# Optimization experiments

Hardware: AMD Instinct MI355X
Metric: run time of the kernel (lower is better)

Reference implementation:

```python
import jax, jax.numpy as jnp
import numpy as np
from jax import lax

BATCH = 2
COUNT = 5
OUT = 125


def _bins(n, out=OUT):
    # PyTorch adaptive_max_pool2d bin boundaries: start=floor(i*n/out), end=ceil((i+1)*n/out)
    i = np.arange(out)
    s = (i * n) // out
    e = -((-(i + 1) * n) // out)
    m = int((e - s).max())
    idx = s[:, None] + np.arange(m)[None, :]
    return np.minimum(idx, n - 1), idx < e[:, None]


def _apool(img):
    # adaptive max pool 2d of [H,W] -> [OUT,OUT]; H,W are concrete Python ints
    H, W = img.shape
    ri, rv = _bins(H)
    ci, cv = _bins(W)
    r = jnp.where(rv[:, :, None], img[ri], -jnp.inf).max(axis=1)       # [OUT, W]
    return jnp.where(cv[None], r[:, ci], -jnp.inf).max(axis=2)         # [OUT, OUT]


def _conv(x, w, b):
    y = lax.conv_general_dilated(x, w, (1, 1), 'VALID', dimension_numbers=('NCHW', 'OIHW', 'NCHW'))
    return y + b[None, :, None, None]


def _bn(x, g, be, m, v):
    inv = g * lax.rsqrt(v + 1e-5)
    return x * inv[None, :, None, None] + (be - m * inv)[None, :, None, None]


def _pool(x, k, s):
    return lax.reduce_window(x, -np.inf, lax.max, (1, 1, k, k), (1, 1, s, s), 'VALID')


def _forward(x, ROI, roi_layer, w1, b1, g1, be1, m1, v1, w2, b2, g2, be2, m2, v2,
             w3, b3, g3, be3, m3, v3, w4, b4, g4, be4, m4, v4, fw1, fb1, fw2, fb2, fw3, fb3):
    ROI = np.asarray(ROI)
    rl = int(roi_layer)
    roiX = jax.nn.relu(_bn(_conv(x, w1, b1), g1, be1, m1, v1))  # [2,3,252,252]
    crops = []
    for k in range(BATCH):
        xs = []
        for j in range(rl):
            for i in range(COUNT):
                y1, y2, x1, x2 = (int(v) for v in ROI[k, i, 0])
                y1 = int(y1 * 0.9); y2 = int(y2 * 0.9); x2 = int(x2 * 0.9); x1 = int(x1 * 0.9)
                xs.append(_apool(roiX[k, j, y1:y2, x1:x2]))
        crops.append(xs)
    # original code prepends each batch's crop list -> batch order reversed; .numpy() detaches grads
    xb = lax.stop_gradient(jnp.stack(crops[1] + crops[0]).reshape(BATCH, COUNT * rl, OUT, OUT))
    norX = _pool(jax.nn.relu(_bn(_conv(x, w2, b2), g2, be2, m2, v2)), 4, 2)  # [2,20,125,125]
    h = jnp.concatenate([norX, xb], axis=1)                                   # [2,35,125,125]
    h = _pool(jax.nn.relu(_bn(_conv(h, w3, b3), g3, be3, m3, v3)), 2, 2)      # [2,50,60,60]
    h = _pool(jax.nn.relu(_bn(_conv(h, w4, b4), g4, be4, m4, v4)), 2, 2)      # [2,25,28,28]
    h = h.reshape(BATCH, -1)                                                  # [2,19600]
    h = jax.nn.relu(h @ fw1 + fb1)
    h = jax.nn.relu(h @ fw2 + fb2)
    h = jax.nn.relu(h @ fw3 + fb3)
    return jax.nn.softmax(h, axis=1)


def setup_inputs() -> dict:
    key = jax.random.key(0)
    ks = jax.random.split(key, 8)
    rng = np.random.default_rng(0)
    y1 = rng.integers(0, 100, (BATCH, COUNT))
    y2 = np.minimum(y1 + rng.integers(60, 150, (BATCH, COUNT)), 251)
    x1 = rng.integers(0, 100, (BATCH, COUNT))
    x2 = np.minimum(x1 + rng.integers(60, 150, (BATCH, COUNT)), 251)
    ROI = jnp.asarray(np.stack([y1, y2, x1, x2], -1)[:, :, None, :].astype(np.int32))
    d = {'x': jax.random.normal(ks[0], (BATCH, 1, 256, 256), jnp.float32), 'ROI': ROI, 'roi_layer': 3}
    d.update(w1=jax.random.normal(ks[1], (3, 1, 5, 5)) * 0.05, b1=jnp.zeros(3), g1=jnp.ones(3), be1=jnp.zeros(3), m1=jnp.zeros(3), v1=jnp.ones(3))
    d.update(w2=jax.random.normal(ks[2], (20, 1, 5, 5)) * 0.05, b2=jnp.zeros(20), g2=jnp.ones(20), be2=jnp.zeros(20), m2=jnp.zeros(20), v2=jnp.ones(20))
    d.update(w3=jax.random.normal(ks[3], (50, 35, 5, 5)) * 0.05, b3=jnp.zeros(50), g3=jnp.ones(50), be3=jnp.zeros(50), m3=jnp.zeros(50), v3=jnp.ones(50))
    d.update(w4=jax.random.normal(ks[4], (25, 50, 5, 5)) * 0.05, b4=jnp.zeros(25), g4=jnp.ones(25), be4=jnp.zeros(25), m4=jnp.zeros(25), v4=jnp.ones(25))
    d.update(fw1=jax.random.normal(ks[5], (25 * 28 * 28, 1024)) * 0.01, fb1=jnp.zeros(1024),
             fw2=jax.random.normal(ks[6], (1024, 32)) * 0.05, fb2=jnp.zeros(32),
             fw3=jax.random.normal(ks[7], (32, 2)) * 0.05, fb3=jnp.zeros(2))
    return d


def reference(x, ROI, roi_layer, w1, b1, g1, be1, m1, v1, w2, b2, g2, be2, m2, v2,
              w3, b3, g3, be3, m3, v3, w4, b4, g4, be4, m4, v4, fw1, fb1, fw2, fb2, fw3, fb3):
    return _forward(x, ROI, roi_layer, w1, b1, g1, be1, m1, v1, w2, b2, g2, be2, m2, v2,
                    w3, b3, g3, be3, m3, v3, w4, b4, g4, be4, m4, v4, fw1, fb1, fw2, fb2, fw3, fb3)
```

## Files before the change

### kernel.cpp

```cpp
#include <hip/hip_runtime.h>
#include <math.h>


#define RL 3
#define NCH 35

__global__ __launch_bounds__(256) void conv2_roi(
    const float* __restrict__ x, const int* __restrict__ ROI,
    const float* __restrict__ w2, const float* __restrict__ b2, const float* __restrict__ g2,
    const float* __restrict__ be2, const float* __restrict__ m2, const float* __restrict__ v2,
    const float* __restrict__ w1, const float* __restrict__ b1, const float* __restrict__ g1,
    const float* __restrict__ be1, const float* __restrict__ m1, const float* __restrict__ v1,
    const float* __restrict__ w3, const float* __restrict__ w4,
    float* __restrict__ wp3, float* __restrict__ wp4,
    float* __restrict__ h1) {
    if (blockIdx.y >= 70) {
        const float* src = (blockIdx.y == 70) ? w3 : w4;
        float* dst = (blockIdx.y == 70) ? wp3 : wp4;
        int rows = (blockIdx.y == 70) ? 50 * 35 : 25 * 50;
        int total = rows * 28;
        for (int i = blockIdx.x * 256 + threadIdx.x; i < total; i += gridDim.x * 256) {
            int t = i % 28, r = i / 28;
            dst[i] = (t < 25) ? src[r * 25 + t] : 0.f;
        }
        return;
    }
    int i = blockIdx.x * 256 + threadIdx.x;
    if (i >= 125 * 125) return;
    int oy = i / 125, ox = i % 125;
    if (blockIdx.y < 40) {
        int c = blockIdx.y % 20;
        int bi = blockIdx.y / 20;
        const float* xp = x + bi * 256 * 256 + (2 * oy) * 256 + 2 * ox;
        float wl[25];
#pragma unroll
        for (int k = 0; k < 25; k++) wl[k] = w2[c * 25 + k];
        float in[8][8];
#pragma unroll
        for (int r = 0; r < 8; r++)
#pragma unroll
            for (int k = 0; k < 4; k++) {
                float2 v2v = *(const float2*)(xp + r * 256 + 2 * k);
                in[r][2 * k] = v2v.x;
                in[r][2 * k + 1] = v2v.y;
            }
        float inv = g2[c] * rsqrtf(v2[c] + 1e-5f);
        float sh = (b2[c] - m2[c]) * inv + be2[c];
        float mx = -INFINITY;
#pragma unroll
        for (int py = 0; py < 4; py++) {
#pragma unroll
            for (int px = 0; px < 4; px++) {
                float acc = 0.f;
#pragma unroll
                for (int ky = 0; ky < 5; ky++)
#pragma unroll
                    for (int kx = 0; kx < 5; kx++)
                        acc = fmaf(in[py + ky][px + kx], wl[ky * 5 + kx], acc);
                mx = fmaxf(mx, fmaxf(acc * inv + sh, 0.f));
            }
        }
        h1[((bi * NCH + c) * 125 + oy) * 125 + ox] = mx;
    } else {
        int yz = blockIdx.y - 40;
        int bi = yz / 15;
        int cc = yz % 15;
        int sb = 1 - bi;
        int j = cc / 5;
        int ri = cc % 5;
        const int* rp = ROI + (sb * 5 + ri) * 4;
        int y1 = (9 * rp[0]) / 10;
        int y2 = (9 * rp[1]) / 10;
        int x1 = (9 * rp[2]) / 10;
        int x2 = (9 * rp[3]) / 10;
        int H = y2 - y1;
        int W = x2 - x1;
        int sy = (oy * H) / 125, ey = ((oy + 1) * H + 124) / 125;
        int sx = (ox * W) / 125, ex = ((ox + 1) * W + 124) / 125;
        float wl[25];
#pragma unroll
        for (int k = 0; k < 25; k++) wl[k] = w1[j * 25 + k];
        float inv = g1[j] * rsqrtf(v1[j] + 1e-5f);
        float sh = (b1[j] - m1[j]) * inv + be1[j];
        const float* xp = x + sb * 256 * 256;
        float mx = -INFINITY;
        for (int r = sy; r < ey; r++) {
            for (int c2 = sx; c2 < ex; c2++) {
                int Y = y1 + r, X = x1 + c2;
                float acc = 0.f;
#pragma unroll
                for (int ky = 0; ky < 5; ky++)
#pragma unroll
                    for (int kx = 0; kx < 5; kx++)
                        acc = fmaf(xp[(Y + ky) * 256 + X + kx], wl[ky * 5 + kx], acc);
                mx = fmaxf(mx, fmaxf(acc * inv + sh, 0.f));
            }
        }
        h1[((bi * NCH + 20 + cc) * 125 + oy) * 125 + ox] = mx;
    }
}

template <int IW, int PO, int CI, int CO, int G, int NG, int NS>
__global__ __launch_bounds__(64, 4) void conv_partial(
    const float* __restrict__ in, const float* __restrict__ wp,
    float* __restrict__ pac) {
    __shared__ float tile[2][20][24];

    const int lane = threadIdx.x;
    const int sy = lane >> 3, sx = lane & 7;
    int z = blockIdx.z;
    const int ng = z % NG; z /= NG;
    const int s = z % NS;
    const int bi = z / NS;
    const int co0 = ng * G;
    constexpr int CPS = (CI + NS - 1) / NS;
    const int ci0 = s * CPS;
    const int ci1 = (ci0 + CPS < CI) ? ci0 + CPS : CI;
    const int px0 = (8 * (int)blockIdx.x < PO - 8) ? 8 * (int)blockIdx.x : PO - 8;
    const int py0 = (8 * (int)blockIdx.y < PO - 8) ? 8 * (int)blockIdx.y : PO - 8;
    const int px = px0 + sx, py = py0 + sy;
    const float* ip = in + (size_t)bi * CI * IW * IW + (size_t)(2 * py0) * IW + 2 * px0;

    int cw[G];
#pragma unroll
    for (int gg = 0; gg < G; gg++) cw[gg] = (co0 + gg < CO) ? co0 + gg : CO - 1;

    float2 sreg[4];
    auto loadstage = [&](int ci) {
        const float* src = ip + (size_t)ci * IW * IW;
#pragma unroll
        for (int k = 0; k < 4; k++) {
            int p = lane + k * 64;
            if (p < 200) {
                int r = p / 10, c2 = (p % 10) * 2;
                sreg[k] = *(const float2*)(src + r * IW + c2);
            }
        }
    };
    auto writestage = [&](int buf) {
#pragma unroll
        for (int k = 0; k < 4; k++) {
            int p = lane + k * 64;
            if (p < 200) {
                int r = p / 10, c2 = (p % 10) * 2;
                *(float2*)&tile[buf][r][c2] = sreg[k];
            }
        }
    };

    float4 wA[7], wB[7];
    auto wload = [&](float4(&wr)[7], int gg, int ci) {
        const float* src = wp + ((size_t)cw[gg] * CI + ci) * 28;
#pragma unroll
        for (int k = 0; k < 7; k++) wr[k] = *(const float4*)(src + 4 * k);
    };

    float acc[G][4];
#pragma unroll
    for (int gg = 0; gg < G; gg++)
#pragma unroll
        for (int q = 0; q < 4; q++) acc[gg][q] = 0.f;

#define WE(W, t) ((t) % 4 == 0 ? W[(t) / 4].x : (t) % 4 == 1 ? W[(t) / 4].y : (t) % 4 == 2 ? W[(t) / 4].z : W[(t) / 4].w)
#define FMAG(W, gg)                                                            \
    {                                                                          \
        _Pragma("unroll") for (int ky = 0; ky < 5; ky++) {                     \
            _Pragma("unroll") for (int kx = 0; kx < 5; kx++) {                 \
                float wv = WE(W, ky * 5 + kx);                                 \
                float e00 = ((kx)&1) ? p[ky][kx >> 1].y : p[ky][kx >> 1].x;    \
                float e01 = ((kx + 1) & 1) ? p[ky][(kx + 1) >> 1].y : p[ky][(kx + 1) >> 1].x; \
                float e10 = ((kx)&1) ? p[ky + 1][kx >> 1].y : p[ky + 1][kx >> 1].x; \
                float e11 = ((kx + 1) & 1) ? p[ky + 1][(kx + 1) >> 1].y : p[ky + 1][(kx + 1) >> 1].x; \
                acc[gg][0] = fmaf(e00, wv, acc[gg][0]);                        \
                acc[gg][1] = fmaf(e01, wv, acc[gg][1]);                        \
                acc[gg][2] = fmaf(e10, wv, acc[gg][2]);                        \
                acc[gg][3] = fmaf(e11, wv, acc[gg][3]);                        \
            }                                                                  \
        }                                                                      \
    }

    loadstage(ci0);
    writestage(0);

    for (int ci = ci0; ci < ci1; ci++) {
        const int cur = (ci - ci0) & 1;
        if (ci + 1 < ci1) loadstage(ci + 1);
        wload(wA, 0, ci);
        float2 p[6][3];
#pragma unroll
        for (int r = 0; r < 6; r++)
#pragma unroll
            for (int c = 0; c < 3; c++)
                p[r][c] = *(const float2*)&tile[cur][2 * sy + r][2 * sx + 2 * c];
        wload(wB, 1, ci);
        FMAG(wA, 0);
        wload(wA, 2, ci);
        FMAG(wB, 1);
        FMAG(wA, 2);
        if (ci + 1 < ci1) writestage(cur ^ 1);
    }
#undef FMAG
#undef WE

    constexpr int CW = 2 * PO;
#pragma unroll
    for (int gg = 0; gg < G; gg++) {
        int co = co0 + gg;
        if (co < CO) {
            size_t base = (((size_t)(s * 2 + bi) * CO + co) * CW + 2 * py) * CW + 2 * px;
            float2 r0 = {acc[gg][0], acc[gg][1]};
            float2 r1 = {acc[gg][2], acc[gg][3]};
            *(float2*)&pac[base] = r0;
            *(float2*)&pac[base + CW] = r1;
        }
    }
}

template <int PO, int CO, int INIT>
__global__ __launch_bounds__(256) void conv_finish(
    const float* __restrict__ pac,
    const float* __restrict__ b, const float* __restrict__ g,
    const float* __restrict__ be, const float* __restrict__ m,
    const float* __restrict__ v, float* __restrict__ out,
    const float* __restrict__ fb1, float* __restrict__ fc1o) {
    int idx = blockIdx.x * 256 + threadIdx.x;
    if (INIT && idx < 2048) fc1o[idx] = fb1[idx & 1023];
    int total = 2 * CO * PO * PO;
    if (idx >= total) return;
    int px = idx % PO;
    int t = idx / PO;
    int py = t % PO; t /= PO;
    int co = t % CO;
    int bi = t / CO;
    constexpr int CW = 2 * PO;
    constexpr size_t SS = (size_t)2 * CO * CW * CW;
    size_t base = (((size_t)bi * CO + co) * CW + 2 * py) * CW + 2 * px;
    float s00 = 0.f, s01 = 0.f, s10 = 0.f, s11 = 0.f;
#pragma unroll
    for (int s = 0; s < 4; s++) {
        float2 a0 = *(const float2*)&pac[base + s * SS];
        float2 a1 = *(const float2*)&pac[base + s * SS + CW];
        s00 += a0.x; s01 += a0.y; s10 += a1.x; s11 += a1.y;
    }
    float inv = g[co] * rsqrtf(v[co] + 1e-5f);
    float sh = (b[co] - m[co]) * inv + be[co];
    float q0 = fmaxf(s00 * inv + sh, 0.f);
    float q1 = fmaxf(s01 * inv + sh, 0.f);
    float q2 = fmaxf(s10 * inv + sh, 0.f);
    float q3 = fmaxf(s11 * inv + sh, 0.f);
    out[idx] = fmaxf(fmaxf(q0, q1), fmaxf(q2, q3));
}

#define CHUNK 50
__global__ void fc1_mm(const float* __restrict__ h, const float* __restrict__ w,
                       float* __restrict__ out) {
    __shared__ float sh[2][CHUNK];
    int o = blockIdx.x * 256 + threadIdx.x;
    int i0 = blockIdx.y * CHUNK;
    if (threadIdx.x < 2 * CHUNK) {
        int r = threadIdx.x / CHUNK, t = threadIdx.x % CHUNK;
        sh[r][t] = h[r * 19600 + i0 + t];
    }
    __syncthreads();
    float a0 = 0.f, a1 = 0.f;
    const float* wp = w + (size_t)i0 * 1024 + o;
#pragma unroll
    for (int i = 0; i < CHUNK; i++) {
        float wv = wp[(size_t)i * 1024];
        a0 = fmaf(sh[0][i], wv, a0);
        a1 = fmaf(sh[1][i], wv, a1);
    }
    atomicAdd(&out[o], a0);
    atomicAdd(&out[1024 + o], a1);
}

__global__ void head(const float* __restrict__ fc1o, const float* __restrict__ fw2,
                     const float* __restrict__ fb2, const float* __restrict__ fw3,
                     const float* __restrict__ fb3, float* __restrict__ out) {
    int bi = blockIdx.x;
    __shared__ float h[1024];
    __shared__ float red[256];
    __shared__ float s2[32];
    for (int i = threadIdx.x; i < 1024; i += 256) h[i] = fmaxf(fc1o[bi * 1024 + i], 0.f);
    __syncthreads();
    int o = threadIdx.x >> 3;
    int part = threadIdx.x & 7;
    float a = 0.f;
    for (int i = part * 128; i < part * 128 + 128; i++) a += h[i] * fw2[i * 32 + o];
    red[threadIdx.x] = a;
    __syncthreads();
    if (part == 0) {
        float s = 0.f;
        for (int p = 0; p < 8; p++) s += red[(o << 3) + p];
        s2[o] = fmaxf(s + fb2[o], 0.f);
    }
    __syncthreads();
    if (threadIdx.x == 0) {
        float z0 = fb3[0], z1 = fb3[1];
        for (int i = 0; i < 32; i++) {
            z0 += s2[i] * fw3[i * 2];
            z1 += s2[i] * fw3[i * 2 + 1];
        }
        z0 = fmaxf(z0, 0.f);
        z1 = fmaxf(z1, 0.f);
        float mx = fmaxf(z0, z1);
        float e0 = expf(z0 - mx), e1 = expf(z1 - mx);
        float s = e0 + e1;
        out[bi * 2 + 0] = e0 / s;
        out[bi * 2 + 1] = e1 / s;
    }
}

extern "C" void kernel_launch(void* const* d_in, const int* in_sizes, int n_in,
                              void* d_out, int out_size, void* d_ws, size_t ws_size,
                              hipStream_t stream) {
    const float* x   = (const float*)d_in[0];
    const int*   ROI = (const int*)d_in[1];
    const float* w1 = (const float*)d_in[3];
    const float* b1 = (const float*)d_in[4];
    const float* g1 = (const float*)d_in[5];
    const float* be1 = (const float*)d_in[6];
    const float* m1 = (const float*)d_in[7];
    const float* v1 = (const float*)d_in[8];
    const float* w2 = (const float*)d_in[9];
    const float* b2 = (const float*)d_in[10];
    const float* g2 = (const float*)d_in[11];
    const float* be2 = (const float*)d_in[12];
    const float* m2 = (const float*)d_in[13];
    const float* v2 = (const float*)d_in[14];
    const float* w3 = (const float*)d_in[15];
    const float* b3 = (const float*)d_in[16];
    const float* g3 = (const float*)d_in[17];
    const float* be3 = (const float*)d_in[18];
    const float* m3 = (const float*)d_in[19];
    const float* v3 = (const float*)d_in[20];
    const float* w4 = (const float*)d_in[21];
    const float* b4 = (const float*)d_in[22];
    const float* g4 = (const float*)d_in[23];
    const float* be4 = (const float*)d_in[24];
    const float* m4 = (const float*)d_in[25];
    const float* v4 = (const float*)d_in[26];
    const float* fw1 = (const float*)d_in[27];
    const float* fb1 = (const float*)d_in[28];
    const float* fw2 = (const float*)d_in[29];
    const float* fb2 = (const float*)d_in[30];
    const float* fw3 = (const float*)d_in[31];
    const float* fb3 = (const float*)d_in[32];
    float* out = (float*)d_out;

    float* ws = (float*)d_ws;
    float* h1   = ws;
    float* p3   = h1 + 1093750;
    float* p4   = p3 + 360000;
    float* fc1o = p4 + 39200;
    float* pac3 = fc1o + 2048;
    float* pac4 = pac3;
    float* wp3  = pac3 + 5760000;
    float* wp4  = wp3 + 49000;

    {
        dim3 grd((125 * 125 + 255) / 256, 72);
        conv2_roi<<<grd, 256, 0, stream>>>(x, ROI, w2, b2, g2, be2, m2, v2,
                                           w1, b1, g1, be1, m1, v1,
                                           w3, w4, wp3, wp4, h1);
    }
    {
        dim3 grd(8, 8, 2 * 4 * 17);
        conv_partial<125, 60, NCH, 50, 3, 17, 4><<<grd, 64, 0, stream>>>(h1, wp3, pac3);
    }
    {
        int total = 2 * 50 * 60 * 60;
        conv_finish<60, 50, 0><<<(total + 255) / 256, 256, 0, stream>>>(
            pac3, b3, g3, be3, m3, v3, p3, nullptr, nullptr);
    }
    {
        dim3 grd(4, 4, 2 * 4 * 9);
        conv_partial<60, 28, 50, 25, 3, 9, 4><<<grd, 64, 0, stream>>>(p3, wp4, pac4);
    }
    {
        int total = 2 * 25 * 28 * 28;
        conv_finish<28, 25, 1><<<(total + 255) / 256, 256, 0, stream>>>(
            pac4, b4, g4, be4, m4, v4, p4, fb1, fc1o);
    }
    {
        dim3 grd(4, 392);
        fc1_mm<<<grd, 256, 0, stream>>>(p4, fw1, fc1o);
    }
    head<<<2, 256, 0, stream>>>(fc1o, fw2, fb2, fw3, fb3, out);
}
```

Baseline: 125.3 us.

## Pad h1 channel stride and software-pipeline conv_partial weight loads across channels

```diff
diff --git a/kernel.cpp b/kernel.cpp
--- a/kernel.cpp
+++ b/kernel.cpp
@@ -4,6 +4,8 @@
 
 #define RL 3
 #define NCH 35
+#define H1C 15626
+#define H1B (35 * H1C)
 
 __global__ __launch_bounds__(256) void conv2_roi(
     const float* __restrict__ x, const int* __restrict__ ROI,
@@ -60,7 +62,7 @@
                 mx = fmaxf(mx, fmaxf(acc * inv + sh, 0.f));
             }
         }
-        h1[((bi * NCH + c) * 125 + oy) * 125 + ox] = mx;
+        h1[(size_t)bi * H1B + (size_t)c * H1C + oy * 125 + ox] = mx;
     } else {
         int yz = blockIdx.y - 40;
         int bi = yz / 15;
@@ -96,12 +98,12 @@
                 mx = fmaxf(mx, fmaxf(acc * inv + sh, 0.f));
             }
         }
-        h1[((bi * NCH + 20 + cc) * 125 + oy) * 125 + ox] = mx;
-    }
-}
-
-template <int IW, int PO, int CI, int CO, int G, int NG, int NS>
-__global__ __launch_bounds__(64, 4) void conv_partial(
+        h1[(size_t)bi * H1B + (size_t)(20 + cc) * H1C + oy * 125 + ox] = mx;
+    }
+}
+
+template <int IW, int PO, int CI, int CO, int G, int NG, int NS, int BST, int CST>
+__global__ __launch_bounds__(64) void conv_partial(
     const float* __restrict__ in, const float* __restrict__ wp,
     float* __restrict__ pac) {
     __shared__ float tile[2][20][24];
@@ -119,7 +121,7 @@
     const int px0 = (8 * (int)blockIdx.x < PO - 8) ? 8 * (int)blockIdx.x : PO - 8;
     const int py0 = (8 * (int)blockIdx.y < PO - 8) ? 8 * (int)blockIdx.y : PO - 8;
     const int px = px0 + sx, py = py0 + sy;
-    const float* ip = in + (size_t)bi * CI * IW * IW + (size_t)(2 * py0) * IW + 2 * px0;
+    const float* ip = in + (size_t)bi * BST + (size_t)(2 * py0) * IW + 2 * px0;
 
     int cw[G];
 #pragma unroll
@@ -127,7 +129,7 @@
 
     float2 sreg[4];
     auto loadstage = [&](int ci) {
-        const float* src = ip + (size_t)ci * IW * IW;
+        const float* src = ip + (size_t)ci * CST;
 #pragma unroll
         for (int k = 0; k < 4; k++) {
             int p = lane + k * 64;
@@ -150,7 +152,8 @@
 
     float4 wA[7], wB[7];
     auto wload = [&](float4(&wr)[7], int gg, int ci) {
-        const float* src = wp + ((size_t)cw[gg] * CI + ci) * 28;
+        int cc = (ci < ci1) ? ci : ci1 - 1;
+        const float* src = wp + ((size_t)cw[gg] * CI + cc) * 28;
 #pragma unroll
         for (int k = 0; k < 7; k++) wr[k] = *(const float4*)(src + 4 * k);
     };
@@ -178,27 +181,42 @@
             }                                                                  \
         }                                                                      \
     }
+#define PREAD(buf)                                                             \
+    float2 p[6][3];                                                            \
+    _Pragma("unroll") for (int r = 0; r < 6; r++)                              \
+        _Pragma("unroll") for (int c = 0; c < 3; c++)                          \
+            p[r][c] = *(const float2*)&tile[buf][2 * sy + r][2 * sx + 2 * c];
 
     loadstage(ci0);
     writestage(0);
-
-    for (int ci = ci0; ci < ci1; ci++) {
-        const int cur = (ci - ci0) & 1;
-        if (ci + 1 < ci1) loadstage(ci + 1);
-        wload(wA, 0, ci);
-        float2 p[6][3];
-#pragma unroll
-        for (int r = 0; r < 6; r++)
-#pragma unroll
-            for (int c = 0; c < 3; c++)
-                p[r][c] = *(const float2*)&tile[cur][2 * sy + r][2 * sx + 2 * c];
-        wload(wB, 1, ci);
-        FMAG(wA, 0);
-        wload(wA, 2, ci);
-        FMAG(wB, 1);
-        FMAG(wA, 2);
-        if (ci + 1 < ci1) writestage(cur ^ 1);
-    }
+    wload(wA, 0, ci0);
+
+#pragma unroll 1
+    for (int ci = ci0; ci < ci1; ci += 2) {
+        {
+            if (ci + 1 < ci1) loadstage(ci + 1);
+            PREAD(0)
+            wload(wB, 1, ci);
+            FMAG(wA, 0);
+            wload(wA, 2, ci);
+            FMAG(wB, 1);
+            wload(wB, 0, ci + 1);
+            FMAG(wA, 2);
+            if (ci + 1 < ci1) writestage(1);
+        }
+        if (ci + 1 < ci1) {
+            if (ci + 2 < ci1) loadstage(ci + 2);
+            PREAD(1)
+            wload(wA, 1, ci + 1);
+            FMAG(wB, 0);
+            wload(wB, 2, ci + 1);
+            FMAG(wA, 1);
+            wload(wA, 0, ci + 2);
+            FMAG(wB, 2);
+            if (ci + 2 < ci1) writestage(0);
+        }
+    }
+#undef PREAD
 #undef FMAG
 #undef WE
 
@@ -350,7 +368,7 @@
 
     float* ws = (float*)d_ws;
     float* h1   = ws;
-    float* p3   = h1 + 1093750;
+    float* p3   = h1 + 2 * H1B;
     float* p4   = p3 + 360000;
     float* fc1o = p4 + 39200;
     float* pac3 = fc1o + 2048;
@@ -366,7 +384,8 @@
     }
     {
         dim3 grd(8, 8, 2 * 4 * 17);
-        conv_partial<125, 60, NCH, 50, 3, 17, 4><<<grd, 64, 0, stream>>>(h1, wp3, pac3);
+        conv_partial<125, 60, NCH, 50, 3, 17, 4, H1B, H1C><<<grd, 64, 0, stream>>>(
+            h1, wp3, pac3);
     }
     {
         int total = 2 * 50 * 60 * 60;
@@ -375,7 +394,8 @@
     }
     {
         dim3 grd(4, 4, 2 * 4 * 9);
-        conv_partial<60, 28, 50, 25, 3, 9, 4><<<grd, 64, 0, stream>>>(p3, wp4, pac4);
+        conv_partial<60, 28, 50, 25, 3, 9, 4, 180000, 3600><<<grd, 64, 0, stream>>>(
+            p3, wp4, pac4);
     }
     {
         int total = 2 * 25 * 28 * 28;
```

After: 125.8 us. About the same (+0.4%).

## Prefetch next-channel weights across conv iterations and pad h1 channel stride

Applied to the files above, without the earlier changes.

```diff
diff --git a/kernel.cpp b/kernel.cpp
--- a/kernel.cpp
+++ b/kernel.cpp
@@ -4,6 +4,8 @@
 
 #define RL 3
 #define NCH 35
+#define H1C 15626
+#define H1B (35 * H1C)
 
 __global__ __launch_bounds__(256) void conv2_roi(
     const float* __restrict__ x, const int* __restrict__ ROI,
@@ -60,7 +62,7 @@
                 mx = fmaxf(mx, fmaxf(acc * inv + sh, 0.f));
             }
         }
-        h1[((bi * NCH + c) * 125 + oy) * 125 + ox] = mx;
+        h1[(size_t)bi * H1B + (size_t)c * H1C + oy * 125 + ox] = mx;
     } else {
         int yz = blockIdx.y - 40;
         int bi = yz / 15;
@@ -96,14 +98,15 @@
                 mx = fmaxf(mx, fmaxf(acc * inv + sh, 0.f));
             }
         }
-        h1[((bi * NCH + 20 + cc) * 125 + oy) * 125 + ox] = mx;
-    }
-}
-
-template <int IW, int PO, int CI, int CO, int G, int NG, int NS>
-__global__ __launch_bounds__(64, 4) void conv_partial(
+        h1[(size_t)bi * H1B + (size_t)(20 + cc) * H1C + oy * 125 + ox] = mx;
+    }
+}
+
+template <int IW, int PO, int CI, int CO, int G, int NG, int NS, int BST, int CST>
+__global__ __launch_bounds__(64) void conv_partial(
     const float* __restrict__ in, const float* __restrict__ wp,
     float* __restrict__ pac) {
+    static_assert(G == 3, "schedule hard-coded for G=3");
     __shared__ float tile[2][20][24];
 
     const int lane = threadIdx.x;
@@ -119,7 +122,7 @@
     const int px0 = (8 * (int)blockIdx.x < PO - 8) ? 8 * (int)blockIdx.x : PO - 8;
     const int py0 = (8 * (int)blockIdx.y < PO - 8) ? 8 * (int)blockIdx.y : PO - 8;
     const int px = px0 + sx, py = py0 + sy;
-    const float* ip = in + (size_t)bi * CI * IW * IW + (size_t)(2 * py0) * IW + 2 * px0;
+    const float* ip = in + (size_t)bi * BST + (size_t)(2 * py0) * IW + 2 * px0;
 
     int cw[G];
 #pragma unroll
@@ -127,7 +130,7 @@
 
     float2 sreg[4];
     auto loadstage = [&](int ci) {
-        const float* src = ip + (size_t)ci * IW * IW;
+        const float* src = ip + (size_t)ci * CST;
 #pragma unroll
         for (int k = 0; k < 4; k++) {
             int p = lane + k * 64;
@@ -148,9 +151,10 @@
         }
     };
 
-    float4 wA[7], wB[7];
+    float4 wA[7], wB[7], wC[7];
     auto wload = [&](float4(&wr)[7], int gg, int ci) {
-        const float* src = wp + ((size_t)cw[gg] * CI + ci) * 28;
+        int cc = (ci < ci1) ? ci : ci1 - 1;
+        const float* src = wp + ((size_t)cw[gg] * CI + cc) * 28;
 #pragma unroll
         for (int k = 0; k < 7; k++) wr[k] = *(const float4*)(src + 4 * k);
     };
@@ -181,23 +185,31 @@
 
     loadstage(ci0);
     writestage(0);
-
+    wload(wA, 0, ci0);
+    wload(wB, 1, ci0);
+    wload(wC, 2, ci0);
+
+#pragma unroll 1
     for (int ci = ci0; ci < ci1; ci++) {
         const int cur = (ci - ci0) & 1;
-        if (ci + 1 < ci1) loadstage(ci + 1);
-        wload(wA, 0, ci);
+        const bool more = (ci + 1 < ci1);
+        if (more) loadstage(ci + 1);
         float2 p[6][3];
 #pragma unroll
         for (int r = 0; r < 6; r++)
 #pragma unroll
             for (int c = 0; c < 3; c++)
                 p[r][c] = *(const float2*)&tile[cur][2 * sy + r][2 * sx + 2 * c];
-        wload(wB, 1, ci);
         FMAG(wA, 0);
-        wload(wA, 2, ci);
+        if (more) wload(wA, 0, ci + 1);
+        __builtin_amdgcn_sched_barrier(0);
         FMAG(wB, 1);
-        FMAG(wA, 2);
-        if (ci + 1 < ci1) writestage(cur ^ 1);
+        if (more) wload(wB, 1, ci + 1);
+        __builtin_amdgcn_sched_barrier(0);
+        FMAG(wC, 2);
+        if (more) wload(wC, 2, ci + 1);
+        __builtin_amdgcn_sched_barrier(0);
+        if (more) writestage(cur ^ 1);
     }
 #undef FMAG
 #undef WE
@@ -350,7 +362,7 @@
 
     float* ws = (float*)d_ws;
     float* h1   = ws;
-    float* p3   = h1 + 1093750;
+    float* p3   = h1 + 2 * H1B;
     float* p4   = p3 + 360000;
     float* fc1o = p4 + 39200;
     float* pac3 = fc1o + 2048;
@@ -366,7 +378,8 @@
     }
     {
         dim3 grd(8, 8, 2 * 4 * 17);
-        conv_partial<125, 60, NCH, 50, 3, 17, 4><<<grd, 64, 0, stream>>>(h1, wp3, pac3);
+        conv_partial<125, 60, NCH, 50, 3, 17, 4, H1B, H1C><<<grd, 64, 0, stream>>>(
+            h1, wp3, pac3);
     }
     {
         int total = 2 * 50 * 60 * 60;
@@ -375,7 +388,8 @@
     }
     {
         dim3 grd(4, 4, 2 * 4 * 9);
-        conv_partial<60, 28, 50, 25, 3, 9, 4><<<grd, 64, 0, stream>>>(p3, wp4, pac4);
+        conv_partial<60, 28, 50, 25, 3, 9, 4, 180000, 3600><<<grd, 64, 0, stream>>>(
+            p3, wp4, pac4);
     }
     {
         int total = 2 * 25 * 28 * 28;
```

Result: slower. 193.0 us (+54.1%).

## Fuse conv4 finish into fc1 and retune conv4 output-channel grouping

Applied to the files above, without the earlier changes.

```diff
diff --git a/kernel.cpp b/kernel.cpp
--- a/kernel.cpp
+++ b/kernel.cpp
@@ -100,10 +100,11 @@
     }
 }
 
-template <int IW, int PO, int CI, int CO, int G, int NG, int NS>
+template <int IW, int PO, int CI, int CO, int G, int NG, int NS, int BST, int CST>
 __global__ __launch_bounds__(64, 4) void conv_partial(
     const float* __restrict__ in, const float* __restrict__ wp,
     float* __restrict__ pac) {
+    static_assert(G == 2 || G == 3, "schedule supports G=2,3");
     __shared__ float tile[2][20][24];
 
     const int lane = threadIdx.x;
@@ -119,7 +120,7 @@
     const int px0 = (8 * (int)blockIdx.x < PO - 8) ? 8 * (int)blockIdx.x : PO - 8;
     const int py0 = (8 * (int)blockIdx.y < PO - 8) ? 8 * (int)blockIdx.y : PO - 8;
     const int px = px0 + sx, py = py0 + sy;
-    const float* ip = in + (size_t)bi * CI * IW * IW + (size_t)(2 * py0) * IW + 2 * px0;
+    const float* ip = in + (size_t)bi * BST + (size_t)(2 * py0) * IW + 2 * px0;
 
     int cw[G];
 #pragma unroll
@@ -127,7 +128,7 @@
 
     float2 sreg[4];
     auto loadstage = [&](int ci) {
-        const float* src = ip + (size_t)ci * IW * IW;
+        const float* src = ip + (size_t)ci * CST;
 #pragma unroll
         for (int k = 0; k < 4; k++) {
             int p = lane + k * 64;
@@ -194,9 +195,13 @@
                 p[r][c] = *(const float2*)&tile[cur][2 * sy + r][2 * sx + 2 * c];
         wload(wB, 1, ci);
         FMAG(wA, 0);
-        wload(wA, 2, ci);
-        FMAG(wB, 1);
-        FMAG(wA, 2);
+        if constexpr (G == 3) {
+            wload(wA, 2, ci);
+            FMAG(wB, 1);
+            FMAG(wA, 2);
+        } else {
+            FMAG(wB, 1);
+        }
         if (ci + 1 < ci1) writestage(cur ^ 1);
     }
 #undef FMAG
@@ -252,14 +257,38 @@
 }
 
 #define CHUNK 50
-__global__ void fc1_mm(const float* __restrict__ h, const float* __restrict__ w,
-                       float* __restrict__ out) {
+__global__ void fc1_mm(const float* __restrict__ pac,
+                       const float* __restrict__ b4, const float* __restrict__ g4,
+                       const float* __restrict__ be4, const float* __restrict__ m4,
+                       const float* __restrict__ v4,
+                       const float* __restrict__ w, float* __restrict__ out) {
     __shared__ float sh[2][CHUNK];
     int o = blockIdx.x * 256 + threadIdx.x;
     int i0 = blockIdx.y * CHUNK;
     if (threadIdx.x < 2 * CHUNK) {
         int r = threadIdx.x / CHUNK, t = threadIdx.x % CHUNK;
-        sh[r][t] = h[r * 19600 + i0 + t];
+        int e = i0 + t;
+        int px = e % 28;
+        int t2 = e / 28;
+        int py = t2 % 28;
+        int co = t2 / 28;
+        const int CW = 56;
+        const int SS = 2 * 25 * CW * CW;
+        int base = ((r * 25 + co) * CW + 2 * py) * CW + 2 * px;
+        float s00 = 0.f, s01 = 0.f, s10 = 0.f, s11 = 0.f;
+#pragma unroll
+        for (int s = 0; s < 4; s++) {
+            float2 a0 = *(const float2*)&pac[base + s * SS];
+            float2 a1 = *(const float2*)&pac[base + s * SS + CW];
+            s00 += a0.x; s01 += a0.y; s10 += a1.x; s11 += a1.y;
+        }
+        float inv = g4[co] * rsqrtf(v4[co] + 1e-5f);
+        float shv = (b4[co] - m4[co]) * inv + be4[co];
+        float q0 = fmaxf(s00 * inv + shv, 0.f);
+        float q1 = fmaxf(s01 * inv + shv, 0.f);
+        float q2 = fmaxf(s10 * inv + shv, 0.f);
+        float q3 = fmaxf(s11 * inv + shv, 0.f);
+        sh[r][t] = fmaxf(fmaxf(q0, q1), fmaxf(q2, q3));
     }
     __syncthreads();
     float a0 = 0.f, a1 = 0.f;
@@ -351,8 +380,7 @@
     float* ws = (float*)d_ws;
     float* h1   = ws;
     float* p3   = h1 + 1093750;
-    float* p4   = p3 + 360000;
-    float* fc1o = p4 + 39200;
+    float* fc1o = p3 + 360000;
     float* pac3 = fc1o + 2048;
     float* pac4 = pac3;
     float* wp3  = pac3 + 5760000;
@@ -366,25 +394,22 @@
     }
     {
         dim3 grd(8, 8, 2 * 4 * 17);
-        conv_partial<125, 60, NCH, 50, 3, 17, 4><<<grd, 64, 0, stream>>>(h1, wp3, pac3);
+        conv_partial<125, 60, NCH, 50, 3, 17, 4, 35 * 15625, 15625>
+            <<<grd, 64, 0, stream>>>(h1, wp3, pac3);
     }
     {
         int total = 2 * 50 * 60 * 60;
-        conv_finish<60, 50, 0><<<(total + 255) / 256, 256, 0, stream>>>(
-            pac3, b3, g3, be3, m3, v3, p3, nullptr, nullptr);
+        conv_finish<60, 50, 1><<<(total + 255) / 256, 256, 0, stream>>>(
+            pac3, b3, g3, be3, m3, v3, p3, fb1, fc1o);
     }
     {
-        dim3 grd(4, 4, 2 * 4 * 9);
-        conv_partial<60, 28, 50, 25, 3, 9, 4><<<grd, 64, 0, stream>>>(p3, wp4, pac4);
-    }
-    {
-        int total = 2 * 25 * 28 * 28;
-        conv_finish<28, 25, 1><<<(total + 255) / 256, 256, 0, stream>>>(
-            pac4, b4, g4, be4, m4, v4, p4, fb1, fc1o);
+        dim3 grd(4, 4, 2 * 4 * 13);
+        conv_partial<60, 28, 50, 25, 2, 13, 4, 180000, 3600>
+            <<<grd, 64, 0, stream>>>(p3, wp4, pac4);
     }
     {
         dim3 grd(4, 392);
-        fc1_mm<<<grd, 256, 0, stream>>>(p4, fw1, fc1o);
+        fc1_mm<<<grd, 256, 0, stream>>>(pac4, b4, g4, be4, m4, v4, fw1, fc1o);
     }
     head<<<2, 256, 0, stream>>>(fc1o, fw2, fb2, fw3, fb3, out);
 }
```

Result: faster. 118.8 us (-5.2%).
